# Optimization experiments

Hardware: AMD Instinct MI355X
Metric: run time of the kernel (lower is better)

The kernel has to match this reference:

```python
import jax, jax.numpy as jnp
import numpy as np

# static config (matches init_kwargs)
E = 1280          # n_embed
L = 4             # n_layer
NH = 16           # n_heads
D = E // NH       # head_dim = 80
M = 5120          # n_mlp
O = 2048          # n_output_embed
MS = 2            # spatial_merge_size
NGPS = 48         # sqrt(num_position_embeddings)
GRID_T, GRID_H, GRID_W = 1, 32, 32
N_IMG = 2
SPP = GRID_T * GRID_H * GRID_W   # 1024 tokens per image
S = N_IMG * SPP                  # 2048 total tokens
H4 = E * MS * MS                 # merger hidden = 5120
IN_PATCH = 3 * 2 * 16 * 16       # 1536
DS_IDX = [1, 2]


def _ln(x, w, b, eps=1e-6):
    m = x.mean(-1, keepdims=True)
    v = ((x - m) ** 2).mean(-1, keepdims=True)
    return (x - m) / jnp.sqrt(v + eps) * w + b


def _pos_embed_interp(pos_emb):
    # bilinear interpolation of the 48x48 learned grid to GRID_HxGRID_W, per image
    hi = jnp.linspace(0.0, NGPS - 1.0, GRID_H)
    wi = jnp.linspace(0.0, NGPS - 1.0, GRID_W)
    hf = hi.astype(jnp.int32); wf = wi.astype(jnp.int32)
    hc = jnp.minimum(hf + 1, NGPS - 1); wc = jnp.minimum(wf + 1, NGPS - 1)
    dh = hi - hf; dw = wi - wf
    idx = [(hf[:, None] * NGPS + wf[None]).ravel(), (hf[:, None] * NGPS + wc[None]).ravel(),
           (hc[:, None] * NGPS + wf[None]).ravel(), (hc[:, None] * NGPS + wc[None]).ravel()]
    wts = [((1 - dh)[:, None] * (1 - dw)[None]).ravel(), ((1 - dh)[:, None] * dw[None]).ravel(),
           (dh[:, None] * (1 - dw)[None]).ravel(), (dh[:, None] * dw[None]).ravel()]
    pe = sum(pos_emb[i] * w[:, None] for i, w in zip(idx, wts))  # [h*w, E]
    pe = jnp.tile(pe, (GRID_T, 1))
    # spatial-merge permutation: (t, h/m, m, w/m, m) -> (t, h/m, w/m, m, m)
    pe = pe.reshape(GRID_T, GRID_H // MS, MS, GRID_W // MS, MS, E).transpose(0, 1, 3, 2, 4, 5).reshape(-1, E)
    return jnp.tile(pe, (N_IMG, 1))  # [S, E]


def _rotary_freqs():
    dim = D // 2  # VisionRotaryEmbedding dim = 40
    inv = 1.0 / (10000.0 ** (jnp.arange(0, dim, 2, dtype=jnp.float32) / dim))  # [D//4]
    hp = jnp.broadcast_to(jnp.arange(GRID_H)[:, None], (GRID_H, GRID_W))
    hp = hp.reshape(GRID_H // MS, MS, GRID_W // MS, MS).transpose(0, 2, 1, 3).ravel()
    wp = jnp.broadcast_to(jnp.arange(GRID_W)[None, :], (GRID_H, GRID_W))
    wp = wp.reshape(GRID_H // MS, MS, GRID_W // MS, MS).transpose(0, 2, 1, 3).ravel()
    pos = jnp.stack([hp, wp], -1)            # [h*w, 2]
    pos = jnp.tile(pos, (GRID_T, 1))
    pos = jnp.tile(pos, (N_IMG, 1))          # [S, 2]
    table = jnp.arange(max(GRID_H, GRID_W), dtype=jnp.float32)[:, None] * inv[None]  # [G, D//4]
    return table[pos].reshape(S, -1)         # [S, D//2] (h-freqs || w-freqs)


def _rope(t, cos, sin):
    # t: [S, NH, D]; cos/sin: [S, 1, D]; applied in float32 as in the source
    t1, t2 = jnp.split(t, 2, axis=-1)
    rot = jnp.concatenate([-t2, t1], -1)
    return (t.astype(jnp.float32) * cos + rot.astype(jnp.float32) * sin).astype(t.dtype)


def _attn(x, qkv_w, qkv_b, pw, pb, cos, sin, mask):
    qkv = (x @ qkv_w.T + qkv_b).reshape(S, 3, NH, D)
    q, k, v = qkv[:, 0], qkv[:, 1], qkv[:, 2]
    q = _rope(q, cos, sin)
    k = _rope(k, cos, sin)
    scores = jnp.einsum('shd,thd->hst', q, k) / np.sqrt(D).astype(np.float32) + mask
    p = jax.nn.softmax(scores.astype(jnp.float32), axis=-1).astype(q.dtype)
    o = jnp.einsum('hst,thd->shd', p, v).reshape(S, E)
    return o @ pw.T + pb


def _merger(x, ln_w, ln_b, f1w, f1b, f2w, f2b, post):
    if post:
        x = _ln(x.reshape(-1, H4), ln_w, ln_b)
    else:
        x = _ln(x, ln_w, ln_b).reshape(-1, H4)
    h = jax.nn.gelu(x @ f1w.T + f1b, approximate=False)  # nn.GELU() exact
    return h @ f2w.T + f2b


def setup_inputs() -> dict:
    key = jax.random.key(0)
    ks = iter(jax.random.split(key, 24))
    n = lambda s: jax.random.normal(next(ks), s, dtype=jnp.float32) * 0.02
    return {
        'x': jax.random.normal(next(ks), (S, IN_PATCH), dtype=jnp.float32),
        'patch_w': n((E, IN_PATCH)), 'patch_b': jnp.zeros((E,), jnp.float32),
        'pos_emb': n((NGPS * NGPS, E)),
        'ln1_w': jnp.ones((L, E), jnp.float32), 'ln1_b': jnp.zeros((L, E), jnp.float32),
        'ln2_w': jnp.ones((L, E), jnp.float32), 'ln2_b': jnp.zeros((L, E), jnp.float32),
        'qkv_w': n((L, 3 * E, E)), 'qkv_b': jnp.zeros((L, 3 * E), jnp.float32),
        'attn_proj_w': n((L, E, E)), 'attn_proj_b': jnp.zeros((L, E), jnp.float32),
        'fc1_w': n((L, M, E)), 'fc1_b': jnp.zeros((L, M), jnp.float32),
        'fc2_w': n((L, E, M)), 'fc2_b': jnp.zeros((L, E), jnp.float32),
        'm_ln_w': jnp.ones((E,), jnp.float32), 'm_ln_b': jnp.zeros((E,), jnp.float32),
        'm_fc1_w': n((H4, H4)), 'm_fc1_b': jnp.zeros((H4,), jnp.float32),
        'm_fc2_w': n((O, H4)), 'm_fc2_b': jnp.zeros((O,), jnp.float32),
        'ds_ln_w': jnp.ones((2, H4), jnp.float32), 'ds_ln_b': jnp.zeros((2, H4), jnp.float32),
        'ds_fc1_w': n((2, H4, H4)), 'ds_fc1_b': jnp.zeros((2, H4), jnp.float32),
        'ds_fc2_w': n((2, O, H4)), 'ds_fc2_b': jnp.zeros((2, O), jnp.float32),
    }


def reference(x, patch_w, patch_b, pos_emb, ln1_w, ln1_b, ln2_w, ln2_b,
              qkv_w, qkv_b, attn_proj_w, attn_proj_b, fc1_w, fc1_b, fc2_w, fc2_b,
              m_ln_w, m_ln_b, m_fc1_w, m_fc1_b, m_fc2_w, m_fc2_b,
              ds_ln_w, ds_ln_b, ds_fc1_w, ds_fc1_b, ds_fc2_w, ds_fc2_b):
    # patch embed (Conv3d with kernel==stride == per-patch linear)
    h = x @ patch_w.T + patch_b                      # [S, E]
    h = h + _pos_embed_interp(pos_emb)
    freqs = _rotary_freqs()                          # [S, D//2]
    cos = jnp.concatenate([jnp.cos(freqs)] * 2, -1)[:, None, :]  # [S,1,D]
    sin = jnp.concatenate([jnp.sin(freqs)] * 2, -1)[:, None, :]
    img = jnp.arange(S) // SPP                       # cu_seqlens block-diagonal mask
    mask = jnp.where(img[:, None] == img[None, :], 0.0, jnp.finfo(jnp.float32).min)
    ds_feats = []
    for l in range(L):
        h = h + _attn(_ln(h, ln1_w[l], ln1_b[l]), qkv_w[l], qkv_b[l],
                      attn_proj_w[l], attn_proj_b[l], cos, sin, mask)
        hn = _ln(h, ln2_w[l], ln2_b[l])
        h = h + (jax.nn.gelu(hn @ fc1_w[l].T + fc1_b[l], approximate=True) @ fc2_w[l].T + fc2_b[l])
        if l in DS_IDX:
            j = DS_IDX.index(l)
            ds_feats.append(_merger(h, ds_ln_w[j], ds_ln_b[j], ds_fc1_w[j], ds_fc1_b[j],
                                    ds_fc2_w[j], ds_fc2_b[j], post=True))
    main = _merger(h, m_ln_w, m_ln_b, m_fc1_w, m_fc1_b, m_fc2_w, m_fc2_b, post=False)
    return jnp.stack([main] + ds_feats, 0)           # [3, S//4, O]
```

## Files before the change

### kernel.cpp

```cpp
#include <hip/hip_runtime.h>
#include <hip/hip_bf16.h>
#include <cstdio>
#include <cstdint>

#define E_    1280
#define L_    4
#define NH_   16
#define D_    80
#define DP_   96
#define MLP_  5120
#define O_    2048
#define S_    2048
#define H4_   5120
#define INP_  1536

typedef __attribute__((ext_vector_type(4))) float f32x4;
typedef __attribute__((ext_vector_type(8))) short short8v;
typedef __attribute__((ext_vector_type(4))) short short4v;

__device__ __forceinline__ short f2bf(float f){
  uint32_t u = __float_as_uint(f);
  uint32_t r = (u + 0x7FFFu + ((u >> 16) & 1u)) >> 16;
  return (short)r;
}
__device__ __forceinline__ float bf2f(short s){
  return __uint_as_float(((uint32_t)(uint16_t)s) << 16);
}
__device__ __forceinline__ float gelu_tanh(float x){
  return 0.5f*x*(1.f + tanhf(0.7978845608028654f*(x + 0.044715f*x*x*x)));
}
__device__ __forceinline__ float gelu_erf(float x){
  return 0.5f*x*(1.f + erff(x*0.7071067811865476f));
}
__device__ __forceinline__ void token_hw(int t, int& hc, int& wc){
  hc = ((t>>1)&1) + ((t>>6)<<1);
  wc = (t&1)      + (((t>>2)&15)<<1);
}

__device__ __forceinline__ void gload16(const short* g, short* l){
  __builtin_amdgcn_global_load_lds((const __attribute__((address_space(1))) void*)g,
                                   (__attribute__((address_space(3))) void*)l, 16, 0, 0);
}

__global__ __launch_bounds__(256)
void cvt_k(const float* __restrict__ src, short* __restrict__ dst, long long n)
{
  const long long stride = (long long)gridDim.x*256*8;
  for (long long i = ((long long)blockIdx.x*256 + threadIdx.x)*8; i < n; i += stride){
    if (i + 8 <= n){
      float4 v0 = *(const float4*)(src+i);
      float4 v1 = *(const float4*)(src+i+4);
      short8v w;
      w[0]=f2bf(v0.x); w[1]=f2bf(v0.y); w[2]=f2bf(v0.z); w[3]=f2bf(v0.w);
      w[4]=f2bf(v1.x); w[5]=f2bf(v1.y); w[6]=f2bf(v1.z); w[7]=f2bf(v1.w);
      *(short8v*)(dst+i) = w;
    } else {
      for (long long j=i;j<n;j++) dst[j] = f2bf(src[j]);
    }
  }
}

struct Gemm2P {
  const short* A; const short* B; void* C;
  const float* bias;
  float* part;
  int lda, ldb, ldc, M, N, K;
  float scale;
  long long aOffH, aOffI, bOffH, bOffI, cOffH, cOffI;
  int nImg, kSplit;
};

template<int EPI, bool RES, bool CF32, bool SPLIT>
__global__ __launch_bounds__(256)
void gemm2_k(Gemm2P p)
{
  __shared__ short As[2][4096];
  __shared__ short Bs[2][4096];

  int z = blockIdx.z, ks = 0;
  if constexpr (SPLIT){ ks = z % p.kSplit; z /= p.kSplit; }
  const int hI = z / p.nImg, iI = z % p.nImg;
  const long long aB = (long long)hI*p.aOffH + (long long)iI*p.aOffI;
  const long long bB = (long long)hI*p.bOffH + (long long)iI*p.bOffI;
  const long long cB = (long long)hI*p.cOffH + (long long)iI*p.cOffI;

  const int nwg = gridDim.x*gridDim.y;
  const int orig = blockIdx.y*gridDim.x + blockIdx.x;
  const int q8 = nwg >> 3, r8 = nwg & 7;
  const int xcd = orig & 7, oidx = orig >> 3;
  const int wg = (xcd < r8 ? xcd*(q8+1) : r8*(q8+1) + (xcd-r8)*q8) + oidx;
  const int nt = wg % gridDim.x, mt = wg / gridDim.x;

  const int tid = threadIdx.x, lane = tid & 63, wv = tid >> 6;

  const int sr = lane >> 2;
  const int sc = (lane & 3) * 8;
  const int Kp  = SPLIT ? p.K / p.kSplit : p.K;
  const int kBeg = SPLIT ? ks * Kp : 0;
  int ra0 = mt*128 + (wv*2+0)*16 + sr; if (ra0 >= p.M) ra0 = p.M-1;
  int ra1 = mt*128 + (wv*2+1)*16 + sr; if (ra1 >= p.M) ra1 = p.M-1;
  int rb0 = nt*128 + (wv*2+0)*16 + sr; if (rb0 >= p.N) rb0 = p.N-1;
  int rb1 = nt*128 + (wv*2+1)*16 + sr; if (rb1 >= p.N) rb1 = p.N-1;
  const short* pa0 = p.A + aB + (long long)ra0*p.lda + sc + kBeg;
  const short* pa1 = p.A + aB + (long long)ra1*p.lda + sc + kBeg;
  const short* pb0 = p.B + bB + (long long)rb0*p.ldb + sc + kBeg;
  const short* pb1 = p.B + bB + (long long)rb1*p.ldb + sc + kBeg;
  const int so0 = (wv*2+0)*512;
  const int so1 = (wv*2+1)*512;

  const int fr = lane & 15, fo = (lane >> 4) * 8;
  const int wr = (wv >> 1) * 64, wc = (wv & 1) * 64;

  f32x4 acc[4][4] = {};

  auto stage = [&](int buf, int k0){
    gload16(pa0 + k0, &As[buf][so0]);
    gload16(pa1 + k0, &As[buf][so1]);
    gload16(pb0 + k0, &Bs[buf][so0]);
    gload16(pb1 + k0, &Bs[buf][so1]);
  };

  const int ntile = Kp >> 5;
  stage(0, 0);
  __syncthreads();
  for (int t = 0; t < ntile; t++){
    const int cur = t & 1;
    if (t + 1 < ntile) stage(cur ^ 1, (t+1) << 5);
    short8v a[4], b[4];
    #pragma unroll
    for (int i=0;i<4;i++){
      a[i] = *(const short8v*)&As[cur][(wr + i*16 + fr)*32 + fo];
      b[i] = *(const short8v*)&Bs[cur][(wc + i*16 + fr)*32 + fo];
    }
    #pragma unroll
    for (int i=0;i<4;i++)
      #pragma unroll
      for (int j=0;j<4;j++)
        acc[i][j] = __builtin_amdgcn_mfma_f32_16x16x32_bf16(a[i], b[j], acc[i][j], 0, 0, 0);
    __syncthreads();
  }

  #pragma unroll
  for (int i=0;i<4;i++){
    #pragma unroll
    for (int j=0;j<4;j++){
      #pragma unroll
      for (int r=0;r<4;r++){
        const int row = mt*128 + wr + i*16 + (lane>>4)*4 + r;
        const int col = nt*128 + wc + j*16 + fr;
        if (row < p.M && col < p.N){
          float v = acc[i][j][r];
          if constexpr (SPLIT){
            p.part[((long long)ks*p.M + row)*p.N + col] = v;
          } else {
            if (p.bias) v += p.bias[col];
            if constexpr (EPI==1) v = gelu_tanh(v);
            if constexpr (EPI==2) v = gelu_erf(v);
            if constexpr (EPI==3) v *= p.scale;
            const long long off = cB + (long long)row*p.ldc + col;
            if constexpr (RES)  v += ((const float*)p.C)[off];
            if constexpr (CF32) ((float*)p.C)[off] = v;
            else                ((short*)p.C)[off] = f2bf(v);
          }
        }
      }
    }
  }
}

template<int EPI, bool RES, bool CF32>
__global__ __launch_bounds__(256)
void reduce_k(const float* __restrict__ part, int kSplit, long long MN, int N,
              const float* __restrict__ bias, void* __restrict__ C)
{
  const long long i = ((long long)blockIdx.x*256 + threadIdx.x)*4;
  if (i >= MN) return;
  float4 s = *(const float4*)(part + i);
  for (int ks = 1; ks < kSplit; ks++){
    const float4 v = *(const float4*)(part + (long long)ks*MN + i);
    s.x += v.x; s.y += v.y; s.z += v.z; s.w += v.w;
  }
  if (bias){
    const int col = (int)(i % N);
    const float4 b = *(const float4*)(bias + col);
    s.x += b.x; s.y += b.y; s.z += b.z; s.w += b.w;
  }
  if constexpr (EPI==1){ s.x=gelu_tanh(s.x); s.y=gelu_tanh(s.y); s.z=gelu_tanh(s.z); s.w=gelu_tanh(s.w); }
  if constexpr (EPI==2){ s.x=gelu_erf(s.x);  s.y=gelu_erf(s.y);  s.z=gelu_erf(s.z);  s.w=gelu_erf(s.w); }
  if constexpr (RES){
    const float4 r = *(const float4*)((const float*)C + i);
    s.x += r.x; s.y += r.y; s.z += r.z; s.w += r.w;
  }
  if constexpr (CF32){
    *(float4*)((float*)C + i) = s;
  } else {
    short4v o; o[0]=f2bf(s.x); o[1]=f2bf(s.y); o[2]=f2bf(s.z); o[3]=f2bf(s.w);
    *(short4v*)((short*)C + i) = o;
  }
}

__global__ __launch_bounds__(256)
void ln_k(const float* __restrict__ X, const float* __restrict__ g, const float* __restrict__ bta,
          short* __restrict__ Y, int Cn)
{
  __shared__ float red[8];
  const int row = blockIdx.x;
  const float* x = X + (long long)row*Cn;
  short* y = Y + (long long)row*Cn;
  float s = 0.f, sq = 0.f;
  for (int c = threadIdx.x*4; c < Cn; c += 1024){
    float4 v = *(const float4*)(x + c);
    s  += v.x+v.y+v.z+v.w;
    sq += v.x*v.x+v.y*v.y+v.z*v.z+v.w*v.w;
  }
  #pragma unroll
  for (int m=32;m;m>>=1){ s += __shfl_xor(s,m,64); sq += __shfl_xor(sq,m,64); }
  const int wv = threadIdx.x>>6, lane = threadIdx.x&63;
  if (lane==0){ red[wv]=s; red[4+wv]=sq; }
  __syncthreads();
  s  = red[0]+red[1]+red[2]+red[3];
  sq = red[4]+red[5]+red[6]+red[7];
  const float mean = s / (float)Cn;
  const float var  = sq / (float)Cn - mean*mean;
  const float rs   = rsqrtf(var + 1e-6f);
  for (int c = threadIdx.x*4; c < Cn; c += 1024){
    float4 v  = *(const float4*)(x + c);
    float4 gw = *(const float4*)(g + c);
    float4 bw = *(const float4*)(bta + c);
    short4v o;
    o[0] = f2bf((v.x-mean)*rs*gw.x + bw.x);
    o[1] = f2bf((v.y-mean)*rs*gw.y + bw.y);
    o[2] = f2bf((v.z-mean)*rs*gw.z + bw.z);
    o[3] = f2bf((v.w-mean)*rs*gw.w + bw.w);
    *(short4v*)(y + c) = o;
  }
}

__global__ __launch_bounds__(256)
void softmax_k(short* __restrict__ P)
{
  __shared__ float red[8];
  const long long row = blockIdx.x;
  short* p = P + row*1024;
  const int tid = threadIdx.x;
  short4v raw = *(short4v*)(p + tid*4);
  float v0=bf2f(raw[0]), v1=bf2f(raw[1]), v2=bf2f(raw[2]), v3=bf2f(raw[3]);
  float mx = fmaxf(fmaxf(v0,v1), fmaxf(v2,v3));
  #pragma unroll
  for (int m=32;m;m>>=1) mx = fmaxf(mx, __shfl_xor(mx,m,64));
  const int wv = tid>>6, lane = tid&63;
  if (lane==0) red[wv]=mx;
  __syncthreads();
  mx = fmaxf(fmaxf(red[0],red[1]), fmaxf(red[2],red[3]));
  __syncthreads();
  v0 = expf(v0-mx); v1 = expf(v1-mx); v2 = expf(v2-mx); v3 = expf(v3-mx);
  float s = v0+v1+v2+v3;
  #pragma unroll
  for (int m=32;m;m>>=1) s += __shfl_xor(s,m,64);
  if (lane==0) red[4+wv]=s;
  __syncthreads();
  s = red[4]+red[5]+red[6]+red[7];
  const float inv = 1.f / s;
  short4v o; o[0]=f2bf(v0*inv); o[1]=f2bf(v1*inv); o[2]=f2bf(v2*inv); o[3]=f2bf(v3*inv);
  *(short4v*)(p + tid*4) = o;
}

__global__ __launch_bounds__(256)
void rope_k(const short* __restrict__ qkv, short* __restrict__ qh,
            short* __restrict__ kh, short* __restrict__ vt)
{
  const int idx = blockIdx.x*256 + threadIdx.x;
  if (idx >= S_*NH_*40) return;
  const int d0 = idx % 40;
  const int h  = (idx / 40) % NH_;
  const int s  = idx / (40*NH_);
  const int t  = s & 1023, img = s >> 10;
  int hc, wc; token_hw(t, hc, wc);
  const int j  = d0 % 20;
  const float invf = exp2f(-0.66438561897747f * (float)j);
  const float pos  = (float)((d0 < 20) ? hc : wc);
  float sn, cs; sincosf(pos * invf, &sn, &cs);
  const short* base = qkv + (long long)s*3840 + h*80;
  const float q1 = bf2f(base[d0]),      q2 = bf2f(base[d0+40]);
  const float k1 = bf2f(base[1280+d0]), k2 = bf2f(base[1280+d0+40]);
  const long long qo = ((long long)h*S_ + s)*DP_;
  qh[qo + d0]    = f2bf(q1*cs - q2*sn);
  qh[qo + d0+40] = f2bf(q2*cs + q1*sn);
  kh[qo + d0]    = f2bf(k1*cs - k2*sn);
  kh[qo + d0+40] = f2bf(k2*cs + k1*sn);
  if (d0 < 16){ qh[qo + 80 + d0] = 0; kh[qo + 80 + d0] = 0; }
  const long long vo = (((long long)h*2 + img)*80)*1024 + t;
  vt[vo + (long long)d0*1024]      = base[2560+d0];
  vt[vo + (long long)(d0+40)*1024] = base[2560+d0+40];
}

__global__ __launch_bounds__(256)
void posadd_k(float* __restrict__ h, const float* __restrict__ pe)
{
  const int idx = blockIdx.x*256 + threadIdx.x;
  if (idx >= S_*(E_/4)) return;
  const int c4 = idx % (E_/4), s = idx / (E_/4);
  const int e = c4*4;
  const int t = s & 1023;
  int hc, wc; token_hw(t, hc, wc);
  const float hi = (float)hc * (47.f/31.f);
  const float wi = (float)wc * (47.f/31.f);
  int hf = (int)hi; float dh = hi - (float)hf; int h2 = min(hf+1, 47);
  int wf = (int)wi; float dw = wi - (float)wf; int w2 = min(wf+1, 47);
  const float w00=(1.f-dh)*(1.f-dw), w01=(1.f-dh)*dw, w10=dh*(1.f-dw), w11=dh*dw;
  const float4 a = *(const float4*)(pe + ((long long)(hf*48+wf))*E_ + e);
  const float4 b = *(const float4*)(pe + ((long long)(hf*48+w2))*E_ + e);
  const float4 c = *(const float4*)(pe + ((long long)(h2*48+wf))*E_ + e);
  const float4 d = *(const float4*)(pe + ((long long)(h2*48+w2))*E_ + e);
  float* out = h + (long long)s*E_ + e;
  float4 o = *(float4*)out;
  o.x += w00*a.x + w01*b.x + w10*c.x + w11*d.x;
  o.y += w00*a.y + w01*b.y + w10*c.y + w11*d.y;
  o.z += w00*a.z + w01*b.z + w10*c.z + w11*d.z;
  o.w += w00*a.w + w01*b.w + w10*c.w + w11*d.w;
  *(float4*)out = o;
}

static Gemm2P mk(const short* A, const short* B, void* C, const float* bias,
                 int lda, int ldb, int ldc, int M, int N, int K, float scale = 1.f)
{
  Gemm2P p{}; p.A=A; p.B=B; p.C=C; p.bias=bias; p.part=nullptr;
  p.lda=lda; p.ldb=ldb; p.ldc=ldc; p.M=M; p.N=N; p.K=K; p.scale=scale;
  p.aOffH=p.aOffI=p.bOffH=p.bOffI=p.cOffH=p.cOffI=0; p.nImg=1; p.kSplit=1;
  return p;
}

extern "C" void kernel_launch(void* const* d_in, const int* in_sizes, int n_in,
                              void* d_out, int out_size, void* d_ws, size_t ws_size,
                              hipStream_t stream)
{
  const float* x           = (const float*)d_in[0];
  const float* patch_w     = (const float*)d_in[1];
  const float* patch_b     = (const float*)d_in[2];
  const float* pos_emb     = (const float*)d_in[3];
  const float* ln1_w       = (const float*)d_in[4];
  const float* ln1_b       = (const float*)d_in[5];
  const float* ln2_w       = (const float*)d_in[6];
  const float* ln2_b       = (const float*)d_in[7];
  const float* qkv_w       = (const float*)d_in[8];
  const float* qkv_b       = (const float*)d_in[9];
  const float* attn_proj_w = (const float*)d_in[10];
  const float* attn_proj_b = (const float*)d_in[11];
  const float* fc1_w       = (const float*)d_in[12];
  const float* fc1_b       = (const float*)d_in[13];
  const float* fc2_w       = (const float*)d_in[14];
  const float* fc2_b       = (const float*)d_in[15];
  const float* m_ln_w      = (const float*)d_in[16];
  const float* m_ln_b      = (const float*)d_in[17];
  const float* m_fc1_w     = (const float*)d_in[18];
  const float* m_fc1_b     = (const float*)d_in[19];
  const float* m_fc2_w     = (const float*)d_in[20];
  const float* m_fc2_b     = (const float*)d_in[21];
  const float* ds_ln_w     = (const float*)d_in[22];
  const float* ds_ln_b     = (const float*)d_in[23];
  const float* ds_fc1_w    = (const float*)d_in[24];
  const float* ds_fc1_b    = (const float*)d_in[25];
  const float* ds_fc2_w    = (const float*)d_in[26];
  const float* ds_fc2_b    = (const float*)d_in[27];
  float* out = (float*)d_out;

  char* wsp = (char*)d_ws;
  auto alloc = [&](size_t bytes)->char*{
    char* p = wsp; wsp += (bytes + 255) & ~(size_t)255; return p;
  };
  float* h    = (float*)alloc((size_t)S_*E_*4);
  short* qkvb = (short*)alloc((size_t)S_*3840*2);
  short* aln  = (short*)alloc((size_t)S_*E_*2);
  short* qh   = (short*)alloc((size_t)NH_*S_*DP_*2);
  short* kh   = (short*)alloc((size_t)NH_*S_*DP_*2);
  short* vt   = (short*)alloc((size_t)NH_*2*D_*1024*2);
  short* p    = (short*)alloc((size_t)NH_*S_*1024*2);
  short* o2   = (short*)alloc((size_t)S_*E_*2);
  short* ffn  = (short*)alloc((size_t)S_*MLP_*2);
  short* xb    = (short*)alloc((size_t)S_*INP_*2);
  short* pwB   = (short*)alloc((size_t)E_*INP_*2);
  short* qkvwB = (short*)alloc((size_t)L_*3840*E_*2);
  short* prwB  = (short*)alloc((size_t)L_*E_*E_*2);
  short* f1wB  = (short*)alloc((size_t)L_*MLP_*E_*2);
  short* f2wB  = (short*)alloc((size_t)L_*E_*MLP_*2);
  short* mf1B  = (short*)alloc((size_t)H4_*H4_*2);
  short* mf2B  = (short*)alloc((size_t)O_*H4_*2);
  short* df1B  = (short*)alloc((size_t)2*H4_*H4_*2);
  short* df2B  = (short*)alloc((size_t)2*O_*H4_*2);
  size_t need = (size_t)(wsp - (char*)d_ws);
  if (need > ws_size){
    fprintf(stderr, "kernel_launch: ws too small: need %zu have %zu\n", need, ws_size);
    return;
  }
  float* part = (float*)p;

  const dim3 B256(256);
  auto cvt = [&](const float* src, short* dst, long long n){
    unsigned blk = (unsigned)min((long long)8192, (n/8 + 255)/256);
    cvt_k<<<blk, B256, 0, stream>>>(src, dst, n);
  };
  cvt(x, xb, (long long)S_*INP_);
  cvt(patch_w, pwB, (long long)E_*INP_);
  cvt(qkv_w, qkvwB, (long long)L_*3840*E_);
  cvt(attn_proj_w, prwB, (long long)L_*E_*E_);
  cvt(fc1_w, f1wB, (long long)L_*MLP_*E_);
  cvt(fc2_w, f2wB, (long long)L_*E_*MLP_);
  cvt(m_fc1_w, mf1B, (long long)H4_*H4_);
  cvt(m_fc2_w, mf2B, (long long)O_*H4_);
  cvt(ds_fc1_w, df1B, (long long)2*H4_*H4_);
  cvt(ds_fc2_w, df2B, (long long)2*O_*H4_);

  auto G = [](int M, int N, int ks = 1){
    return dim3((unsigned)((N+127)/128), (unsigned)((M+127)/128), (unsigned)ks);
  };
  auto RG = [](long long MN){ return dim3((unsigned)((MN/4 + 255)/256)); };

  { Gemm2P pp = mk(xb, pwB, h, nullptr, INP_, INP_, E_, S_, E_, INP_);
    pp.part = part; pp.kSplit = 4;
    gemm2_k<0,false,true,true><<<G(S_,E_,4),B256,0,stream>>>(pp);
    reduce_k<0,false,true><<<RG((long long)S_*E_),B256,0,stream>>>(part, 4, (long long)S_*E_, E_, patch_b, h); }
  posadd_k<<<(S_*(E_/4)+255)/256, B256, 0, stream>>>(h, pos_emb);

  for (int l = 0; l < L_; l++){
    ln_k<<<S_, B256, 0, stream>>>(h, ln1_w + l*E_, ln1_b + l*E_, aln, E_);
    { Gemm2P pp = mk(aln, qkvwB + (size_t)l*3840*E_, qkvb, qkv_b + l*3840, E_, E_, 3840, S_, 3840, E_);
      gemm2_k<0,false,false,false><<<G(S_,3840),B256,0,stream>>>(pp); }
    rope_k<<<(S_*NH_*40+255)/256, B256, 0, stream>>>(qkvb, qh, kh, vt);
    { Gemm2P pp = mk(qh, kh, p, nullptr, DP_, DP_, 1024, 1024, 1024, DP_, 0.11180339887498949f);
      pp.aOffH=(long long)S_*DP_; pp.aOffI=(long long)1024*DP_;
      pp.bOffH=(long long)S_*DP_; pp.bOffI=(long long)1024*DP_;
      pp.cOffH=(long long)S_*1024; pp.cOffI=(long long)1024*1024; pp.nImg=2;
      gemm2_k<3,false,false,false><<<dim3(8,8,32),B256,0,stream>>>(pp); }
    softmax_k<<<NH_*S_, B256, 0, stream>>>(p);
    { Gemm2P pp = mk(p, vt, o2, nullptr, 1024, 1024, E_, 1024, D_, 1024);
      pp.aOffH=(long long)S_*1024; pp.aOffI=(long long)1024*1024;
      pp.bOffH=(long long)2*D_*1024; pp.bOffI=(long long)D_*1024;
      pp.cOffH=D_; pp.cOffI=(long long)1024*E_; pp.nImg=2;
      gemm2_k<0,false,false,false><<<dim3(1,8,32),B256,0,stream>>>(pp); }
    { Gemm2P pp = mk(o2, prwB + (size_t)l*E_*E_, h, nullptr, E_, E_, E_, S_, E_, E_);
      pp.part = part; pp.kSplit = 4;
      gemm2_k<0,false,true,true><<<G(S_,E_,4),B256,0,stream>>>(pp);
      reduce_k<0,true,true><<<RG((long long)S_*E_),B256,0,stream>>>(part, 4, (long long)S_*E_, E_, attn_proj_b + l*E_, h); }

    ln_k<<<S_, B256, 0, stream>>>(h, ln2_w + l*E_, ln2_b + l*E_, aln, E_);
    { Gemm2P pp = mk(aln, f1wB + (size_t)l*MLP_*E_, ffn, fc1_b + l*MLP_, E_, E_, MLP_, S_, MLP_, E_);
      gemm2_k<1,false,false,false><<<G(S_,MLP_),B256,0,stream>>>(pp); }
    { Gemm2P pp = mk(ffn, f2wB + (size_t)l*E_*MLP_, h, nullptr, MLP_, MLP_, E_, S_, E_, MLP_);
      pp.part = part; pp.kSplit = 4;
      gemm2_k<0,false,true,true><<<G(S_,E_,4),B256,0,stream>>>(pp);
      reduce_k<0,true,true><<<RG((long long)S_*E_),B256,0,stream>>>(part, 4, (long long)S_*E_, E_, fc2_b + l*E_, h); }

    if (l == 1 || l == 2){
      const int j = l - 1;
      ln_k<<<512, B256, 0, stream>>>(h, ds_ln_w + (size_t)j*H4_, ds_ln_b + (size_t)j*H4_, aln, H4_);
      { Gemm2P pp = mk(aln, df1B + (size_t)j*H4_*H4_, ffn, nullptr, H4_, H4_, H4_, 512, H4_, H4_);
        pp.part = part; pp.kSplit = 4;
        gemm2_k<0,false,false,true><<<G(512,H4_,4),B256,0,stream>>>(pp);
        reduce_k<2,false,false><<<RG((long long)512*H4_),B256,0,stream>>>(part, 4, (long long)512*H4_, H4_, ds_fc1_b + (size_t)j*H4_, ffn); }
      { Gemm2P pp = mk(ffn, df2B + (size_t)j*O_*H4_, out + (size_t)(1+j)*512*O_, nullptr, H4_, H4_, O_, 512, O_, H4_);
        pp.part = part; pp.kSplit = 8;
        gemm2_k<0,false,true,true><<<G(512,O_,8),B256,0,stream>>>(pp);
        reduce_k<0,false,true><<<RG((long long)512*O_),B256,0,stream>>>(part, 8, (long long)512*O_, O_, ds_fc2_b + (size_t)j*O_, out + (size_t)(1+j)*512*O_); }
    }
  }

  ln_k<<<S_, B256, 0, stream>>>(h, m_ln_w, m_ln_b, aln, E_);
  { Gemm2P pp = mk(aln, mf1B, ffn, nullptr, H4_, H4_, H4_, 512, H4_, H4_);
    pp.part = part; pp.kSplit = 4;
    gemm2_k<0,false,false,true><<<G(512,H4_,4),B256,0,stream>>>(pp);
    reduce_k<2,false,false><<<RG((long long)512*H4_),B256,0,stream>>>(part, 4, (long long)512*H4_, H4_, m_fc1_b, ffn); }
  { Gemm2P pp = mk(ffn, mf2B, out, nullptr, H4_, H4_, O_, 512, O_, H4_);
    pp.part = part; pp.kSplit = 8;
    gemm2_k<0,false,true,true><<<G(512,O_,8),B256,0,stream>>>(pp);
    reduce_k<0,false,true><<<RG((long long)512*O_),B256,0,stream>>>(part, 8, (long long)512*O_, O_, m_fc2_b, out); }
}
```

Measured before the change: 1.805 ms.

## Fuse attention into a flash-attention kernel and triple-buffer GEMM loads

Replaces the QK^T GEMM, separate softmax kernel and PV GEMM with a single flash-style kernel. It keeps scores in registers and LDS with an online softmax, so the 16x2048x1024 probability matrix never goes through global memory. Separately, the GEMM mainloop moves from double to triple buffering with explicit vmcnt waits and a single barrier per tile, so loads run further ahead. The costs are more LDS per block, which may lower occupancy, and only 256 attention workgroups per layer.

```diff
diff --git a/kernel.cpp b/kernel.cpp
--- a/kernel.cpp
+++ b/kernel.cpp
@@ -74,8 +74,8 @@
 __global__ __launch_bounds__(256)
 void gemm2_k(Gemm2P p)
 {
-  __shared__ short As[2][4096];
-  __shared__ short Bs[2][4096];
+  __shared__ short As[3][4096];
+  __shared__ short Bs[3][4096];
 
   int z = blockIdx.z, ks = 0;
   if constexpr (SPLIT){ ks = z % p.kSplit; z /= p.kSplit; }
@@ -113,7 +113,8 @@
 
   f32x4 acc[4][4] = {};
 
-  auto stage = [&](int buf, int k0){
+  auto stage = [&](int buf, int t){
+    const int k0 = t << 5;
     gload16(pa0 + k0, &As[buf][so0]);
     gload16(pa1 + k0, &As[buf][so1]);
     gload16(pb0 + k0, &Bs[buf][so0]);
@@ -122,10 +123,13 @@
 
   const int ntile = Kp >> 5;
   stage(0, 0);
-  __syncthreads();
+  if (ntile > 1) stage(1, 1);
   for (int t = 0; t < ntile; t++){
-    const int cur = t & 1;
-    if (t + 1 < ntile) stage(cur ^ 1, (t+1) << 5);
+    const int cur = t % 3;
+    if (t + 1 < ntile) { asm volatile("s_waitcnt vmcnt(4)" ::: "memory"); }
+    else               { asm volatile("s_waitcnt vmcnt(0)" ::: "memory"); }
+    __builtin_amdgcn_s_barrier();
+    asm volatile("" ::: "memory");
     short8v a[4], b[4];
     #pragma unroll
     for (int i=0;i<4;i++){
@@ -137,7 +141,7 @@
       #pragma unroll
       for (int j=0;j<4;j++)
         acc[i][j] = __builtin_amdgcn_mfma_f32_16x16x32_bf16(a[i], b[j], acc[i][j], 0, 0, 0);
-    __syncthreads();
+    if (t + 2 < ntile) stage((t+2)%3, t+2);
   }
 
   #pragma unroll
@@ -200,6 +204,149 @@
 }
 
 __global__ __launch_bounds__(256)
+void fattn_k(const short* __restrict__ qh, const short* __restrict__ kh,
+             const short* __restrict__ vt, short* __restrict__ o2)
+{
+  __shared__ short Ks[2][13312];
+  __shared__ short Vs[2][12288];
+  __shared__ short Ps[17408];
+
+  const int qt = blockIdx.x, h = blockIdx.y, img = blockIdx.z;
+  const int tid = threadIdx.x, lane = tid & 63, wv = tid >> 6;
+  const int fr = lane & 15, fo = (lane >> 4) * 8, g = lane >> 4;
+  const int wr = wv * 32;
+
+  const short* qp = qh + ((long long)h*S_ + img*1024 + qt*128)*DP_;
+  const short* kp = kh + ((long long)h*S_ + img*1024)*DP_;
+  const short* vp = vt + ((long long)(h*2 + img))*80*1024;
+
+  short8v q[2][3];
+  #pragma unroll
+  for (int i=0;i<2;i++)
+    #pragma unroll
+    for (int t3=0;t3<3;t3++)
+      q[i][t3] = *(const short8v*)(qp + (long long)(wr + i*16 + fr)*DP_ + t3*32 + fo);
+
+  int rK[7], cK[7], rV[6], cV[6];
+  #pragma unroll
+  for (int it=0; it<7; it++){
+    const int o = it*4096 + tid*16;
+    int r = o / 208, c = o % 208;
+    if (c >= 192) c = 0;
+    rK[it] = r; cK[it] = c >> 1;
+  }
+  #pragma unroll
+  for (int it=0; it<6; it++){
+    const int o = it*4096 + tid*16;
+    int r = o / 304, c = o % 304;
+    if (r >= 80){ r = 0; c = 0; }
+    if (c >= 256) c = 0;
+    rV[it] = r; cV[it] = c >> 1;
+  }
+
+  auto stage = [&](int b, int t){
+    #pragma unroll
+    for (int it=0; it<7; it++)
+      if (it*4 + wv < 26)
+        gload16(kp + (long long)(t*128 + rK[it])*DP_ + cK[it], &Ks[b][it*2048 + wv*512]);
+    #pragma unroll
+    for (int it=0; it<6; it++)
+      gload16(vp + (long long)rV[it]*1024 + t*128 + cV[it], &Vs[b][it*2048 + wv*512]);
+  };
+
+  float m_[2][4], l_[2][4];
+  f32x4 ao[2][5] = {};
+  #pragma unroll
+  for (int i=0;i<2;i++)
+    #pragma unroll
+    for (int r=0;r<4;r++){ m_[i][r] = -3.0e38f; l_[i][r] = 0.f; }
+
+  stage(0, 0);
+  __syncthreads();
+
+  for (int t = 0; t < 8; t++){
+    const int b = t & 1;
+    if (t < 7) stage(b^1, t+1);
+
+    f32x4 sc[2][8] = {};
+    #pragma unroll
+    for (int j=0;j<8;j++){
+      #pragma unroll
+      for (int t3=0;t3<3;t3++){
+        const short8v kb = *(const short8v*)&Ks[b][(j*16+fr)*104 + t3*32 + fo];
+        sc[0][j] = __builtin_amdgcn_mfma_f32_16x16x32_bf16(q[0][t3], kb, sc[0][j], 0,0,0);
+        sc[1][j] = __builtin_amdgcn_mfma_f32_16x16x32_bf16(q[1][t3], kb, sc[1][j], 0,0,0);
+      }
+    }
+    #pragma unroll
+    for (int i=0;i<2;i++)
+      #pragma unroll
+      for (int j=0;j<8;j++)
+        sc[i][j] *= 0.11180339887498949f;
+
+    #pragma unroll
+    for (int i=0;i<2;i++){
+      #pragma unroll
+      for (int r=0;r<4;r++){
+        float mx = sc[i][0][r];
+        #pragma unroll
+        for (int j=1;j<8;j++) mx = fmaxf(mx, sc[i][j][r]);
+        mx = fmaxf(mx, __shfl_xor(mx, 1, 64));
+        mx = fmaxf(mx, __shfl_xor(mx, 2, 64));
+        mx = fmaxf(mx, __shfl_xor(mx, 4, 64));
+        mx = fmaxf(mx, __shfl_xor(mx, 8, 64));
+        const float mn = fmaxf(m_[i][r], mx);
+        const float al = __expf(m_[i][r] - mn);
+        float ts = 0.f;
+        #pragma unroll
+        for (int j=0;j<8;j++){
+          const float pv = __expf(sc[i][j][r] - mn);
+          sc[i][j][r] = pv;
+          ts += pv;
+        }
+        ts += __shfl_xor(ts, 1, 64);
+        ts += __shfl_xor(ts, 2, 64);
+        ts += __shfl_xor(ts, 4, 64);
+        ts += __shfl_xor(ts, 8, 64);
+        l_[i][r] = l_[i][r]*al + ts;
+        m_[i][r] = mn;
+        #pragma unroll
+        for (int n=0;n<5;n++) ao[i][n][r] *= al;
+        const int row = wr + i*16 + g*4 + r;
+        #pragma unroll
+        for (int j=0;j<8;j++) Ps[row*136 + j*16 + fr] = f2bf(sc[i][j][r]);
+      }
+    }
+
+    #pragma unroll
+    for (int t4=0;t4<4;t4++){
+      short8v pa0 = *(const short8v*)&Ps[(wr + 0  + fr)*136 + t4*32 + fo];
+      short8v pa1 = *(const short8v*)&Ps[(wr + 16 + fr)*136 + t4*32 + fo];
+      #pragma unroll
+      for (int n=0;n<5;n++){
+        const short8v vb = *(const short8v*)&Vs[b][(n*16+fr)*152 + t4*32 + fo];
+        ao[0][n] = __builtin_amdgcn_mfma_f32_16x16x32_bf16(pa0, vb, ao[0][n], 0,0,0);
+        ao[1][n] = __builtin_amdgcn_mfma_f32_16x16x32_bf16(pa1, vb, ao[1][n], 0,0,0);
+      }
+    }
+    __syncthreads();
+  }
+
+  short* op = o2 + ((long long)(img*1024 + qt*128))*E_ + h*80;
+  #pragma unroll
+  for (int i=0;i<2;i++){
+    #pragma unroll
+    for (int r=0;r<4;r++){
+      const float inv = 1.f / l_[i][r];
+      const int row = wr + i*16 + g*4 + r;
+      #pragma unroll
+      for (int n=0;n<5;n++)
+        op[(long long)row*E_ + n*16 + fr] = f2bf(ao[i][n][r] * inv);
+    }
+  }
+}
+
+__global__ __launch_bounds__(256)
 void ln_k(const float* __restrict__ X, const float* __restrict__ g, const float* __restrict__ bta,
           short* __restrict__ Y, int Cn)
 {
@@ -234,35 +381,6 @@
     o[3] = f2bf((v.w-mean)*rs*gw.w + bw.w);
     *(short4v*)(y + c) = o;
   }
-}
-
-__global__ __launch_bounds__(256)
-void softmax_k(short* __restrict__ P)
-{
-  __shared__ float red[8];
-  const long long row = blockIdx.x;
-  short* p = P + row*1024;
-  const int tid = threadIdx.x;
-  short4v raw = *(short4v*)(p + tid*4);
-  float v0=bf2f(raw[0]), v1=bf2f(raw[1]), v2=bf2f(raw[2]), v3=bf2f(raw[3]);
-  float mx = fmaxf(fmaxf(v0,v1), fmaxf(v2,v3));
-  #pragma unroll
-  for (int m=32;m;m>>=1) mx = fmaxf(mx, __shfl_xor(mx,m,64));
-  const int wv = tid>>6, lane = tid&63;
-  if (lane==0) red[wv]=mx;
-  __syncthreads();
-  mx = fmaxf(fmaxf(red[0],red[1]), fmaxf(red[2],red[3]));
-  __syncthreads();
-  v0 = expf(v0-mx); v1 = expf(v1-mx); v2 = expf(v2-mx); v3 = expf(v3-mx);
-  float s = v0+v1+v2+v3;
-  #pragma unroll
-  for (int m=32;m;m>>=1) s += __shfl_xor(s,m,64);
-  if (lane==0) red[4+wv]=s;
-  __syncthreads();
-  s = red[4]+red[5]+red[6]+red[7];
-  const float inv = 1.f / s;
-  short4v o; o[0]=f2bf(v0*inv); o[1]=f2bf(v1*inv); o[2]=f2bf(v2*inv); o[3]=f2bf(v3*inv);
-  *(short4v*)(p + tid*4) = o;
 }
 
 __global__ __launch_bounds__(256)
@@ -372,9 +490,9 @@
   short* qkvb = (short*)alloc((size_t)S_*3840*2);
   short* aln  = (short*)alloc((size_t)S_*E_*2);
   short* qh   = (short*)alloc((size_t)NH_*S_*DP_*2);
-  short* kh   = (short*)alloc((size_t)NH_*S_*DP_*2);
-  short* vt   = (short*)alloc((size_t)NH_*2*D_*1024*2);
-  short* p    = (short*)alloc((size_t)NH_*S_*1024*2);
+  short* kh   = (short*)alloc((size_t)NH_*S_*DP_*2 + 4096);
+  short* vt   = (short*)alloc((size_t)NH_*2*D_*1024*2 + 4096);
+  float* part = (float*)alloc((size_t)48*1024*1024);
   short* o2   = (short*)alloc((size_t)S_*E_*2);
   short* ffn  = (short*)alloc((size_t)S_*MLP_*2);
   short* xb    = (short*)alloc((size_t)S_*INP_*2);
@@ -392,7 +510,6 @@
     fprintf(stderr, "kernel_launch: ws too small: need %zu have %zu\n", need, ws_size);
     return;
   }
-  float* part = (float*)p;
 
   const dim3 B256(256);
   auto cvt = [&](const float* src, short* dst, long long n){
@@ -426,17 +543,7 @@
     { Gemm2P pp = mk(aln, qkvwB + (size_t)l*3840*E_, qkvb, qkv_b + l*3840, E_, E_, 3840, S_, 3840, E_);
       gemm2_k<0,false,false,false><<<G(S_,3840),B256,0,stream>>>(pp); }
     rope_k<<<(S_*NH_*40+255)/256, B256, 0, stream>>>(qkvb, qh, kh, vt);
-    { Gemm2P pp = mk(qh, kh, p, nullptr, DP_, DP_, 1024, 1024, 1024, DP_, 0.11180339887498949f);
-      pp.aOffH=(long long)S_*DP_; pp.aOffI=(long long)1024*DP_;
-      pp.bOffH=(long long)S_*DP_; pp.bOffI=(long long)1024*DP_;
-      pp.cOffH=(long long)S_*1024; pp.cOffI=(long long)1024*1024; pp.nImg=2;
-      gemm2_k<3,false,false,false><<<dim3(8,8,32),B256,0,stream>>>(pp); }
-    softmax_k<<<NH_*S_, B256, 0, stream>>>(p);
-    { Gemm2P pp = mk(p, vt, o2, nullptr, 1024, 1024, E_, 1024, D_, 1024);
-      pp.aOffH=(long long)S_*1024; pp.aOffI=(long long)1024*1024;
-      pp.bOffH=(long long)2*D_*1024; pp.bOffI=(long long)D_*1024;
-      pp.cOffH=D_; pp.cOffI=(long long)1024*E_; pp.nImg=2;
-      gemm2_k<0,false,false,false><<<dim3(1,8,32),B256,0,stream>>>(pp); }
+    fattn_k<<<dim3(8,16,2), B256, 0, stream>>>(qh, kh, vt, o2);
     { Gemm2P pp = mk(o2, prwB + (size_t)l*E_*E_, h, nullptr, E_, E_, E_, S_, E_, E_);
       pp.part = part; pp.kSplit = 4;
       gemm2_k<0,false,true,true><<<G(S_,E_,4),B256,0,stream>>>(pp);
```

Result: faster. 1.635 ms (-9.4%).
